# Kernel optimization log

Hardware: AMD Instinct MI355X
Metric: run time of the kernel (lower is better)

Reference implementation:

```python
import jax, jax.numpy as jnp
import numpy as np

B, C, H, W = 4, 64, 128, 128
HEADS, DIM_HEAD = 8, 64
INNER = HEADS * DIM_HEAD
EPS = 1e-12  # torch F.normalize default eps


def setup_inputs() -> dict:
    key = jax.random.key(0)
    ks = jax.random.split(key, 6)
    s_in = 1.0 / np.sqrt(C)
    s_pr = 1.0 / np.sqrt(INNER)
    return {
        "x_in": jax.random.normal(ks[0], (B, C, H, W), dtype=jnp.float32),
        "Wq": jax.random.uniform(ks[1], (C, INNER), jnp.float32, -s_in, s_in),
        "Wk": jax.random.uniform(ks[2], (C, INNER), jnp.float32, -s_in, s_in),
        "Wv": jax.random.uniform(ks[3], (C, INNER), jnp.float32, -s_in, s_in),
        "Wp": jax.random.uniform(ks[4], (INNER, C), jnp.float32, -s_pr, s_pr),
        "bp": jax.random.uniform(ks[5], (C,), jnp.float32, -s_pr, s_pr),
        "rescale": jnp.ones((HEADS, 1, 1), dtype=jnp.float32),
    }


def _l2norm(t):
    # normalize along last axis (the token axis n), matching F.normalize(p=2)
    n = jnp.sqrt(jnp.sum(t * t, axis=-1, keepdims=True))
    return t / jnp.maximum(n, EPS)


def reference(x_in, Wq, Wk, Wv, Wp, bp, rescale):
    b, c, h, w = x_in.shape
    n = h * w
    x = x_in.transpose(0, 2, 3, 1).reshape(b, n, c)  # [b, n, c]

    def heads_first(t):  # [b, n, inner] -> [b, heads, d, n]
        return t.reshape(b, n, HEADS, DIM_HEAD).transpose(0, 2, 3, 1)

    q = _l2norm(heads_first(x @ Wq))  # [b, H, d, n]
    k = _l2norm(heads_first(x @ Wk))
    v = heads_first(x @ Wv)

    # channel-channel attention: attn[d, e] = sum_n k[d, n] * q[e, n]
    attn = jnp.einsum('bhdn,bhen->bhde', k, q) * rescale  # [b, H, d, d]
    attn = jax.nn.softmax(attn, axis=-1)

    o = jnp.einsum('bhde,bhen->bhdn', attn, v)            # [b, H, d, n]
    o = o.transpose(0, 3, 1, 2).reshape(b, n, INNER)      # [b, n, inner]
    out = (o @ Wp + bp).reshape(b, h, w, c).transpose(0, 3, 1, 2)  # [b, c, h, w]
    return out, attn
```

## Files before the change

kernel.cpp:

```cpp
#include <hip/hip_runtime.h>
#include <math.h>

#define BB 4
#define CC 64
#define NN 16384
#define HEADS 8
#define INNER 512

__global__ __launch_bounds__(256) void k_gram(const float* __restrict__ x,
                                              float* __restrict__ part,
                                              int nslice) {
    const int s = blockIdx.x, b = blockIdx.y;
    const int t = threadIdx.x;
    const int g = t >> 6, lane = t & 63;
    const int rg = lane >> 4;
    const int r0 = g * 16 + rg * 4;
    const int c0 = (lane & 15) * 4;
    __shared__ float xs[64][68];
    float acc[4][4];
#pragma unroll
    for (int i = 0; i < 4; i++)
#pragma unroll
        for (int j = 0; j < 4; j++) acc[i][j] = 0.f;

    const float* xb = x + (size_t)b * CC * NN;
    const int cols = NN / nslice;
    const int ntiles = cols >> 6;
    const int nbase = s * cols;
    for (int tile = 0; tile < ntiles; ++tile) {
        const int n0 = nbase + tile * 64;
#pragma unroll
        for (int k = 0; k < 4; k++) {
            int f = k * 256 + t;
            int c = f >> 4, j4 = f & 15;
            const float4 v = *reinterpret_cast<const float4*>(xb + (size_t)c * NN + n0 + j4 * 4);
            xs[j4 * 4 + 0][c] = v.x; xs[j4 * 4 + 1][c] = v.y;
            xs[j4 * 4 + 2][c] = v.z; xs[j4 * 4 + 3][c] = v.w;
        }
        __syncthreads();
#pragma unroll 8
        for (int n = 0; n < 64; ++n) {
            const float4 a4 = *reinterpret_cast<const float4*>(&xs[n][r0]);
            const float4 b4 = *reinterpret_cast<const float4*>(&xs[n][c0]);
            acc[0][0] = fmaf(a4.x, b4.x, acc[0][0]); acc[0][1] = fmaf(a4.x, b4.y, acc[0][1]);
            acc[0][2] = fmaf(a4.x, b4.z, acc[0][2]); acc[0][3] = fmaf(a4.x, b4.w, acc[0][3]);
            acc[1][0] = fmaf(a4.y, b4.x, acc[1][0]); acc[1][1] = fmaf(a4.y, b4.y, acc[1][1]);
            acc[1][2] = fmaf(a4.y, b4.z, acc[1][2]); acc[1][3] = fmaf(a4.y, b4.w, acc[1][3]);
            acc[2][0] = fmaf(a4.z, b4.x, acc[2][0]); acc[2][1] = fmaf(a4.z, b4.y, acc[2][1]);
            acc[2][2] = fmaf(a4.z, b4.z, acc[2][2]); acc[2][3] = fmaf(a4.z, b4.w, acc[2][3]);
            acc[3][0] = fmaf(a4.w, b4.x, acc[3][0]); acc[3][1] = fmaf(a4.w, b4.y, acc[3][1]);
            acc[3][2] = fmaf(a4.w, b4.z, acc[3][2]); acc[3][3] = fmaf(a4.w, b4.w, acc[3][3]);
        }
        __syncthreads();
    }
    float* p = part + (size_t)(b * nslice + s) * 4096;
#pragma unroll
    for (int i = 0; i < 4; i++) {
        float4 v; v.x = acc[i][0]; v.y = acc[i][1]; v.z = acc[i][2]; v.w = acc[i][3];
        *reinterpret_cast<float4*>(p + (r0 + i) * 64 + c0) = v;
    }
}

__global__ __launch_bounds__(256) void k_redG(const float* __restrict__ part,
                                              float* __restrict__ G,
                                              int nslice) {
    const int b = blockIdx.y;
    const int idx = blockIdx.x * 256 + threadIdx.x;
    const float* p = part + (size_t)b * nslice * 4096 + idx;
    float s0 = 0.f, s1 = 0.f, s2 = 0.f, s3 = 0.f;
    for (int s = 0; s < nslice; s += 4) {
        s0 += p[(size_t)s * 4096];
        s1 += p[(size_t)(s + 1) * 4096];
        s2 += p[(size_t)(s + 2) * 4096];
        s3 += p[(size_t)(s + 3) * 4096];
    }
    G[(size_t)b * 4096 + idx] = (s0 + s1) + (s2 + s3);
}

__global__ __launch_bounds__(256) void k_attn(const float* __restrict__ G,
                                              const float* __restrict__ Wq,
                                              const float* __restrict__ Wk,
                                              const float* __restrict__ Wv,
                                              const float* __restrict__ Wp,
                                              const float* __restrict__ rescale,
                                              float* __restrict__ attn_out,
                                              float* __restrict__ Mg) {
    const int bh = blockIdx.x;
    const int b = bh >> 3, h = bh & 7;
    const int t = threadIdx.x;
    const int ti = t >> 4, tj = t & 15;
    __shared__ float Gs[64][68], Ws[64][68], Ts[64][68];
    __shared__ float qn[64], kn[64];

    for (int k = 0; k < 16; k++) { int f = k * 256 + t; Gs[f >> 6][f & 63] = G[(size_t)b * 4096 + f]; }
    for (int k = 0; k < 16; k++) { int f = k * 256 + t; int c = f >> 6, e = f & 63;
        Ws[c][e] = Wq[(size_t)c * INNER + h * 64 + e]; }
    __syncthreads();

    {
        float acc[4][4] = {};
        for (int k2 = 0; k2 < 64; k2++) {
            const float4 a4 = *reinterpret_cast<const float4*>(&Gs[k2][ti * 4]);
            const float4 b4 = *reinterpret_cast<const float4*>(&Ws[k2][tj * 4]);
            float a[4] = {a4.x, a4.y, a4.z, a4.w}, bv[4] = {b4.x, b4.y, b4.z, b4.w};
#pragma unroll
            for (int i = 0; i < 4; i++)
#pragma unroll
                for (int j = 0; j < 4; j++) acc[i][j] = fmaf(a[i], bv[j], acc[i][j]);
        }
#pragma unroll
        for (int i = 0; i < 4; i++)
#pragma unroll
            for (int j = 0; j < 4; j++) Ts[ti * 4 + i][tj * 4 + j] = acc[i][j];
    }
    __syncthreads();
    if (t < 64) {
        float s = 0.f;
        for (int c = 0; c < 64; c++) s += Ws[c][t] * Ts[c][t];
        qn[t] = fmaxf(sqrtf(s), 1e-12f);
    }
    __syncthreads();
    for (int k = 0; k < 16; k++) { int f = k * 256 + t; int c = f >> 6, e = f & 63;
        Ws[c][e] = Wk[(size_t)c * INNER + h * 64 + e]; }
    __syncthreads();

    float S[4][4] = {};
    for (int k2 = 0; k2 < 64; k2++) {
        const float4 a4 = *reinterpret_cast<const float4*>(&Ws[k2][ti * 4]);
        const float4 b4 = *reinterpret_cast<const float4*>(&Ts[k2][tj * 4]);
        float a[4] = {a4.x, a4.y, a4.z, a4.w}, bv[4] = {b4.x, b4.y, b4.z, b4.w};
#pragma unroll
        for (int i = 0; i < 4; i++)
#pragma unroll
            for (int j = 0; j < 4; j++) S[i][j] = fmaf(a[i], bv[j], S[i][j]);
    }

    {
        float acc[4][4] = {};
        for (int k2 = 0; k2 < 64; k2++) {
            const float4 a4 = *reinterpret_cast<const float4*>(&Gs[k2][ti * 4]);
            const float4 b4 = *reinterpret_cast<const float4*>(&Ws[k2][tj * 4]);
            float a[4] = {a4.x, a4.y, a4.z, a4.w}, bv[4] = {b4.x, b4.y, b4.z, b4.w};
#pragma unroll
            for (int i = 0; i < 4; i++)
#pragma unroll
                for (int j = 0; j < 4; j++) acc[i][j] = fmaf(a[i], bv[j], acc[i][j]);
        }
        __syncthreads();
#pragma unroll
        for (int i = 0; i < 4; i++)
#pragma unroll
            for (int j = 0; j < 4; j++) Ts[ti * 4 + i][tj * 4 + j] = acc[i][j];
    }
    __syncthreads();
    if (t < 64) {
        float s = 0.f;
        for (int c = 0; c < 64; c++) s += Ws[c][t] * Ts[c][t];
        kn[t] = fmaxf(sqrtf(s), 1e-12f);
    }
    __syncthreads();

    const float resc = rescale[h];
    float qinv[4];
#pragma unroll
    for (int j = 0; j < 4; j++) qinv[j] = 1.f / qn[tj * 4 + j];
    float p[4][4];
#pragma unroll
    for (int i = 0; i < 4; i++) {
        const float ki = resc / kn[ti * 4 + i];
        float m = -3.402823466e+38f;
#pragma unroll
        for (int j = 0; j < 4; j++) {
            float L = S[i][j] * ki * qinv[j];
            p[i][j] = L;
            m = fmaxf(m, L);
        }
        for (int o = 1; o < 16; o <<= 1) m = fmaxf(m, __shfl_xor(m, o, 64));
        float ssum = 0.f;
#pragma unroll
        for (int j = 0; j < 4; j++) { p[i][j] = expf(p[i][j] - m); ssum += p[i][j]; }
        for (int o = 1; o < 16; o <<= 1) ssum += __shfl_xor(ssum, o, 64);
        const float inv = 1.f / ssum;
#pragma unroll
        for (int j = 0; j < 4; j++) p[i][j] *= inv;
    }

    float* ao = attn_out + (size_t)bh * 64 * 64;
#pragma unroll
    for (int i = 0; i < 4; i++) {
        float4 v; v.x = p[i][0]; v.y = p[i][1]; v.z = p[i][2]; v.w = p[i][3];
        *reinterpret_cast<float4*>(ao + (size_t)(ti * 4 + i) * 64 + tj * 4) = v;
#pragma unroll
        for (int j = 0; j < 4; j++) Ts[tj * 4 + j][ti * 4 + i] = p[i][j];
    }
    for (int k = 0; k < 16; k++) { int f = k * 256 + t; int c = f >> 6, e = f & 63;
        Ws[e][c] = Wv[(size_t)c * INNER + h * 64 + e]; }
    __syncthreads();

    float accv[4][4] = {};
    for (int e = 0; e < 64; e++) {
        const float4 a4 = *reinterpret_cast<const float4*>(&Ws[e][ti * 4]);
        const float4 b4 = *reinterpret_cast<const float4*>(&Ts[e][tj * 4]);
        float a[4] = {a4.x, a4.y, a4.z, a4.w}, bv[4] = {b4.x, b4.y, b4.z, b4.w};
#pragma unroll
        for (int i = 0; i < 4; i++)
#pragma unroll
            for (int j = 0; j < 4; j++) accv[i][j] = fmaf(a[i], bv[j], accv[i][j]);
    }
    __syncthreads();
#pragma unroll
    for (int i = 0; i < 4; i++)
#pragma unroll
        for (int j = 0; j < 4; j++) Ts[tj * 4 + j][ti * 4 + i] = accv[i][j];
    for (int k = 0; k < 16; k++) { int f = k * 256 + t;
        Ws[f >> 6][f & 63] = Wp[(size_t)h * 4096 + f]; }
    __syncthreads();

    float accm[4][4] = {};
    for (int d = 0; d < 64; d++) {
        const float4 a4 = *reinterpret_cast<const float4*>(&Ts[d][ti * 4]);
        const float4 b4 = *reinterpret_cast<const float4*>(&Ws[d][tj * 4]);
        float a[4] = {a4.x, a4.y, a4.z, a4.w}, bv[4] = {b4.x, b4.y, b4.z, b4.w};
#pragma unroll
        for (int i = 0; i < 4; i++)
#pragma unroll
            for (int j = 0; j < 4; j++) accm[i][j] = fmaf(a[i], bv[j], accm[i][j]);
    }
    float* Mb = Mg + (size_t)b * 4096;
#pragma unroll
    for (int i = 0; i < 4; i++)
#pragma unroll
        for (int j = 0; j < 4; j++)
            atomicAdd(&Mb[(ti * 4 + i) * 64 + tj * 4 + j], accm[i][j]);
}

__global__ __launch_bounds__(256) void k_out(const float* __restrict__ x,
                                             const float* __restrict__ Mg,
                                             const float* __restrict__ bp,
                                             float* __restrict__ out) {
    const int sn = blockIdx.x, b = blockIdx.y;
    const int t = threadIdx.x, ti = t >> 4, tj = t & 15;
    __shared__ float Ms[64][68], xs[64][68];
    for (int k = 0; k < 16; k++) { int f = k * 256 + t; Ms[f >> 6][f & 63] = Mg[(size_t)b * 4096 + f]; }
    const int n0 = sn * 64;
    const float* xb = x + (size_t)b * CC * NN;
#pragma unroll
    for (int k = 0; k < 4; k++) {
        int f = k * 256 + t; int c = f >> 4, j4 = f & 15;
        float4 v = *reinterpret_cast<const float4*>(xb + (size_t)c * NN + n0 + j4 * 4);
        xs[c][j4 * 4 + 0] = v.x; xs[c][j4 * 4 + 1] = v.y;
        xs[c][j4 * 4 + 2] = v.z; xs[c][j4 * 4 + 3] = v.w;
    }
    __syncthreads();
    float acc[4][4];
#pragma unroll
    for (int i = 0; i < 4; i++) {
        const float bv = bp[ti * 4 + i];
#pragma unroll
        for (int j = 0; j < 4; j++) acc[i][j] = bv;
    }
    for (int c = 0; c < 64; c++) {
        const float4 m4 = *reinterpret_cast<const float4*>(&Ms[c][ti * 4]);
        const float4 x4 = *reinterpret_cast<const float4*>(&xs[c][tj * 4]);
        float m[4] = {m4.x, m4.y, m4.z, m4.w}, xv[4] = {x4.x, x4.y, x4.z, x4.w};
#pragma unroll
        for (int i = 0; i < 4; i++)
#pragma unroll
            for (int j = 0; j < 4; j++) acc[i][j] = fmaf(m[i], xv[j], acc[i][j]);
    }
    float* ob = out + (size_t)b * CC * NN;
#pragma unroll
    for (int i = 0; i < 4; i++) {
        float4 v; v.x = acc[i][0]; v.y = acc[i][1]; v.z = acc[i][2]; v.w = acc[i][3];
        *reinterpret_cast<float4*>(ob + (size_t)(ti * 4 + i) * NN + n0 + tj * 4) = v;
    }
}

extern "C" void kernel_launch(void* const* d_in, const int* in_sizes, int n_in,
                              void* d_out, int out_size, void* d_ws, size_t ws_size,
                              hipStream_t stream) {
    const float* x  = (const float*)d_in[0];
    const float* Wq = (const float*)d_in[1];
    const float* Wk = (const float*)d_in[2];
    const float* Wv = (const float*)d_in[3];
    const float* Wp = (const float*)d_in[4];
    const float* bp = (const float*)d_in[5];
    const float* rescale = (const float*)d_in[6];
    float* out = (float*)d_out;
    float* attn_out = out + (size_t)BB * CC * NN;
    float* ws = (float*)d_ws;

    const size_t fixed_floats = (size_t)BB * 4096
                              + (size_t)BB * 4096;
    int nslice = 256;
    while (nslice > 4 &&
           ((size_t)BB * nslice * 4096 + fixed_floats) * sizeof(float) > ws_size)
        nslice >>= 1;

    float* part = ws;
    float* G    = part + (size_t)BB * nslice * 4096;
    float* Mg   = G + (size_t)BB * 4096;

    hipMemsetAsync(Mg, 0, (size_t)BB * 4096 * sizeof(float), stream);
    hipLaunchKernelGGL(k_gram,  dim3(nslice, BB),  dim3(256), 0, stream, x, part, nslice);
    hipLaunchKernelGGL(k_redG,  dim3(16, BB),      dim3(256), 0, stream, part, G, nslice);
    hipLaunchKernelGGL(k_attn,  dim3(BB * HEADS),  dim3(256), 0, stream, G, Wq, Wk, Wv, Wp, rescale, attn_out, Mg);
    hipLaunchKernelGGL(k_out,   dim3(NN / 64, BB), dim3(256), 0, stream, x, Mg, bp, out);
}
```

Measured before the change: 137.6 us.

## Fold Gram reduction into atomics and split attention blocks by row quarter

The Gram kernel now uses a fixed 64 slices per batch and accumulates its partial results straight into G with atomicAdd, which removes the partial buffer and the separate reduction kernel. The attention kernel is split four ways per (batch, head): each block computes 16 rows of the attention matrix and their share of the fused Wv·attn·Wp product, then adds that share into M atomically. Weights are loaded up front with vectorized loads. This cuts a launch and the workspace traffic and gives 128 attention blocks instead of 32, in exchange for redundant Tq/Gs work per quarter, more atomic contention, and a Gram sum order that is no longer deterministic.

New measurement: 143.2 us. +4.1%, slower.

```diff
diff --git a/kernel.cpp b/kernel.cpp
--- a/kernel.cpp
+++ b/kernel.cpp
@@ -6,10 +6,10 @@
 #define NN 16384
 #define HEADS 8
 #define INNER 512
+#define NSLICE 64
 
 __global__ __launch_bounds__(256) void k_gram(const float* __restrict__ x,
-                                              float* __restrict__ part,
-                                              int nslice) {
+                                              float* __restrict__ G) {
     const int s = blockIdx.x, b = blockIdx.y;
     const int t = threadIdx.x;
     const int g = t >> 6, lane = t & 63;
@@ -24,10 +24,8 @@
         for (int j = 0; j < 4; j++) acc[i][j] = 0.f;
 
     const float* xb = x + (size_t)b * CC * NN;
-    const int cols = NN / nslice;
-    const int ntiles = cols >> 6;
-    const int nbase = s * cols;
-    for (int tile = 0; tile < ntiles; ++tile) {
+    const int nbase = s * (NN / NSLICE);
+    for (int tile = 0; tile < (NN / NSLICE) / 64; ++tile) {
         const int n0 = nbase + tile * 64;
 #pragma unroll
         for (int k = 0; k < 4; k++) {
@@ -53,28 +51,12 @@
         }
         __syncthreads();
     }
-    float* p = part + (size_t)(b * nslice + s) * 4096;
-#pragma unroll
-    for (int i = 0; i < 4; i++) {
-        float4 v; v.x = acc[i][0]; v.y = acc[i][1]; v.z = acc[i][2]; v.w = acc[i][3];
-        *reinterpret_cast<float4*>(p + (r0 + i) * 64 + c0) = v;
-    }
-}
-
-__global__ __launch_bounds__(256) void k_redG(const float* __restrict__ part,
-                                              float* __restrict__ G,
-                                              int nslice) {
-    const int b = blockIdx.y;
-    const int idx = blockIdx.x * 256 + threadIdx.x;
-    const float* p = part + (size_t)b * nslice * 4096 + idx;
-    float s0 = 0.f, s1 = 0.f, s2 = 0.f, s3 = 0.f;
-    for (int s = 0; s < nslice; s += 4) {
-        s0 += p[(size_t)s * 4096];
-        s1 += p[(size_t)(s + 1) * 4096];
-        s2 += p[(size_t)(s + 2) * 4096];
-        s3 += p[(size_t)(s + 3) * 4096];
-    }
-    G[(size_t)b * 4096 + idx] = (s0 + s1) + (s2 + s3);
+    float* Gb = G + (size_t)b * 4096;
+#pragma unroll
+    for (int i = 0; i < 4; i++)
+#pragma unroll
+        for (int j = 0; j < 4; j++)
+            atomicAdd(&Gb[(r0 + i) * 64 + c0 + j], acc[i][j]);
 }
 
 __global__ __launch_bounds__(256) void k_attn(const float* __restrict__ G,
@@ -85,18 +67,48 @@
                                               const float* __restrict__ rescale,
                                               float* __restrict__ attn_out,
                                               float* __restrict__ Mg) {
-    const int bh = blockIdx.x;
+    const int quad = blockIdx.x & 3;
+    const int bh = blockIdx.x >> 2;
     const int b = bh >> 3, h = bh & 7;
+    const int d0g = quad * 16;
     const int t = threadIdx.x;
+
+    __shared__ float Gs[64][68];
+    __shared__ float Tq[64][68];
+    __shared__ float Ws[64][68];
+    __shared__ float WkQ[64][20];
+    __shared__ float Atn[64][20];
+    __shared__ float qn[64], kn[16];
+
+#pragma unroll
+    for (int k = 0; k < 4; k++) {
+        int idx = k * 1024 + t * 4;
+        int r = idx >> 6, c = idx & 63;
+        float4 v = *reinterpret_cast<const float4*>(G + (size_t)b * 4096 + idx);
+        *reinterpret_cast<float4*>(&Gs[r][c]) = v;
+        float4 w = *reinterpret_cast<const float4*>(Wq + (size_t)r * INNER + h * 64 + c);
+        *reinterpret_cast<float4*>(&Ws[r][c]) = w;
+    }
+    {
+        int c = t >> 2, dl = (t & 3) * 4;
+        float4 v = *reinterpret_cast<const float4*>(Wk + (size_t)c * INNER + h * 64 + d0g + dl);
+        *reinterpret_cast<float4*>(&WkQ[c][dl]) = v;
+    }
+    float4 wvr[4];
+#pragma unroll
+    for (int k = 0; k < 4; k++) {
+        int idx = k * 1024 + t * 4;
+        int r = idx >> 6, c = idx & 63;
+        wvr[k] = *reinterpret_cast<const float4*>(Wv + (size_t)r * INNER + h * 64 + c);
+    }
+    float4 wpr;
+    {
+        int dl = t >> 4, c2 = (t & 15) * 4;
+        wpr = *reinterpret_cast<const float4*>(Wp + (size_t)(h * 64 + d0g + dl) * 64 + c2);
+    }
+    __syncthreads();
+
     const int ti = t >> 4, tj = t & 15;
-    __shared__ float Gs[64][68], Ws[64][68], Ts[64][68];
-    __shared__ float qn[64], kn[64];
-
-    for (int k = 0; k < 16; k++) { int f = k * 256 + t; Gs[f >> 6][f & 63] = G[(size_t)b * 4096 + f]; }
-    for (int k = 0; k < 16; k++) { int f = k * 256 + t; int c = f >> 6, e = f & 63;
-        Ws[c][e] = Wq[(size_t)c * INNER + h * 64 + e]; }
-    __syncthreads();
-
     {
         float acc[4][4] = {};
         for (int k2 = 0; k2 < 64; k2++) {
@@ -109,129 +121,121 @@
                 for (int j = 0; j < 4; j++) acc[i][j] = fmaf(a[i], bv[j], acc[i][j]);
         }
 #pragma unroll
-        for (int i = 0; i < 4; i++)
-#pragma unroll
-            for (int j = 0; j < 4; j++) Ts[ti * 4 + i][tj * 4 + j] = acc[i][j];
-    }
-    __syncthreads();
+        for (int i = 0; i < 4; i++) {
+            float4 v; v.x = acc[i][0]; v.y = acc[i][1]; v.z = acc[i][2]; v.w = acc[i][3];
+            *reinterpret_cast<float4*>(&Tq[ti * 4 + i][tj * 4]) = v;
+        }
+    }
+    {
+        const int c = t >> 2, dl0 = (t & 3) * 4;
+        float tk[4] = {};
+        for (int k = 0; k < 64; k++) {
+            const float a = Gs[k][c];
+            const float4 b4 = *reinterpret_cast<const float4*>(&WkQ[k][dl0]);
+            tk[0] = fmaf(a, b4.x, tk[0]); tk[1] = fmaf(a, b4.y, tk[1]);
+            tk[2] = fmaf(a, b4.z, tk[2]); tk[3] = fmaf(a, b4.w, tk[3]);
+        }
+        float4 v; v.x = tk[0]; v.y = tk[1]; v.z = tk[2]; v.w = tk[3];
+        *reinterpret_cast<float4*>(&Atn[c][dl0]) = v;
+    }
+    __syncthreads();
+
+    {
+        const int e = t >> 2, sub = t & 3;
+        float s = 0.f;
+        for (int c = sub * 16; c < sub * 16 + 16; c++) s += Ws[c][e] * Tq[c][e];
+        s += __shfl_xor(s, 1, 64);
+        s += __shfl_xor(s, 2, 64);
+        if (sub == 0) qn[e] = fmaxf(sqrtf(s), 1e-12f);
+    }
     if (t < 64) {
+        const int dl = t >> 2, sub = t & 3;
         float s = 0.f;
-        for (int c = 0; c < 64; c++) s += Ws[c][t] * Ts[c][t];
-        qn[t] = fmaxf(sqrtf(s), 1e-12f);
-    }
-    __syncthreads();
-    for (int k = 0; k < 16; k++) { int f = k * 256 + t; int c = f >> 6, e = f & 63;
-        Ws[c][e] = Wk[(size_t)c * INNER + h * 64 + e]; }
-    __syncthreads();
-
-    float S[4][4] = {};
-    for (int k2 = 0; k2 < 64; k2++) {
-        const float4 a4 = *reinterpret_cast<const float4*>(&Ws[k2][ti * 4]);
-        const float4 b4 = *reinterpret_cast<const float4*>(&Ts[k2][tj * 4]);
-        float a[4] = {a4.x, a4.y, a4.z, a4.w}, bv[4] = {b4.x, b4.y, b4.z, b4.w};
-#pragma unroll
-        for (int i = 0; i < 4; i++)
-#pragma unroll
-            for (int j = 0; j < 4; j++) S[i][j] = fmaf(a[i], bv[j], S[i][j]);
-    }
-
-    {
-        float acc[4][4] = {};
-        for (int k2 = 0; k2 < 64; k2++) {
-            const float4 a4 = *reinterpret_cast<const float4*>(&Gs[k2][ti * 4]);
-            const float4 b4 = *reinterpret_cast<const float4*>(&Ws[k2][tj * 4]);
-            float a[4] = {a4.x, a4.y, a4.z, a4.w}, bv[4] = {b4.x, b4.y, b4.z, b4.w};
-#pragma unroll
-            for (int i = 0; i < 4; i++)
-#pragma unroll
-                for (int j = 0; j < 4; j++) acc[i][j] = fmaf(a[i], bv[j], acc[i][j]);
-        }
-        __syncthreads();
-#pragma unroll
-        for (int i = 0; i < 4; i++)
-#pragma unroll
-            for (int j = 0; j < 4; j++) Ts[ti * 4 + i][tj * 4 + j] = acc[i][j];
-    }
-    __syncthreads();
-    if (t < 64) {
-        float s = 0.f;
-        for (int c = 0; c < 64; c++) s += Ws[c][t] * Ts[c][t];
-        kn[t] = fmaxf(sqrtf(s), 1e-12f);
+        for (int c = sub * 16; c < sub * 16 + 16; c++) s += WkQ[c][dl] * Atn[c][dl];
+        s += __shfl_xor(s, 1, 64);
+        s += __shfl_xor(s, 2, 64);
+        if (sub == 0) kn[dl] = fmaxf(sqrtf(s), 1e-12f);
+    }
+    const int d = t >> 4, e0 = (t & 15) * 4;
+    float s4[4] = {};
+    for (int c = 0; c < 64; c++) {
+        const float a = WkQ[c][d];
+        const float4 b4 = *reinterpret_cast<const float4*>(&Tq[c][e0]);
+        s4[0] = fmaf(a, b4.x, s4[0]); s4[1] = fmaf(a, b4.y, s4[1]);
+        s4[2] = fmaf(a, b4.z, s4[2]); s4[3] = fmaf(a, b4.w, s4[3]);
     }
     __syncthreads();
 
     const float resc = rescale[h];
-    float qinv[4];
-#pragma unroll
-    for (int j = 0; j < 4; j++) qinv[j] = 1.f / qn[tj * 4 + j];
-    float p[4][4];
-#pragma unroll
-    for (int i = 0; i < 4; i++) {
-        const float ki = resc / kn[ti * 4 + i];
+    float p[4];
+    {
+        const float ki = resc / kn[d];
         float m = -3.402823466e+38f;
 #pragma unroll
         for (int j = 0; j < 4; j++) {
-            float L = S[i][j] * ki * qinv[j];
-            p[i][j] = L;
-            m = fmaxf(m, L);
+            p[j] = s4[j] * ki / qn[e0 + j];
+            m = fmaxf(m, p[j]);
         }
         for (int o = 1; o < 16; o <<= 1) m = fmaxf(m, __shfl_xor(m, o, 64));
         float ssum = 0.f;
 #pragma unroll
-        for (int j = 0; j < 4; j++) { p[i][j] = expf(p[i][j] - m); ssum += p[i][j]; }
+        for (int j = 0; j < 4; j++) { p[j] = expf(p[j] - m); ssum += p[j]; }
         for (int o = 1; o < 16; o <<= 1) ssum += __shfl_xor(ssum, o, 64);
         const float inv = 1.f / ssum;
 #pragma unroll
-        for (int j = 0; j < 4; j++) p[i][j] *= inv;
-    }
-
-    float* ao = attn_out + (size_t)bh * 64 * 64;
-#pragma unroll
-    for (int i = 0; i < 4; i++) {
-        float4 v; v.x = p[i][0]; v.y = p[i][1]; v.z = p[i][2]; v.w = p[i][3];
-        *reinterpret_cast<float4*>(ao + (size_t)(ti * 4 + i) * 64 + tj * 4) = v;
-#pragma unroll
-        for (int j = 0; j < 4; j++) Ts[tj * 4 + j][ti * 4 + i] = p[i][j];
-    }
-    for (int k = 0; k < 16; k++) { int f = k * 256 + t; int c = f >> 6, e = f & 63;
-        Ws[e][c] = Wv[(size_t)c * INNER + h * 64 + e]; }
-    __syncthreads();
-
-    float accv[4][4] = {};
-    for (int e = 0; e < 64; e++) {
-        const float4 a4 = *reinterpret_cast<const float4*>(&Ws[e][ti * 4]);
-        const float4 b4 = *reinterpret_cast<const float4*>(&Ts[e][tj * 4]);
-        float a[4] = {a4.x, a4.y, a4.z, a4.w}, bv[4] = {b4.x, b4.y, b4.z, b4.w};
+        for (int j = 0; j < 4; j++) p[j] *= inv;
+    }
+    {
+        float4 v; v.x = p[0]; v.y = p[1]; v.z = p[2]; v.w = p[3];
+        *reinterpret_cast<float4*>(attn_out + (size_t)bh * 4096 + (size_t)(d0g + d) * 64 + e0) = v;
+#pragma unroll
+        for (int j = 0; j < 4; j++) Atn[e0 + j][d] = p[j];
+    }
+#pragma unroll
+    for (int k = 0; k < 4; k++) {
+        int idx = k * 1024 + t * 4;
+        int r = idx >> 6, c = idx & 63;
+        *reinterpret_cast<float4*>(&Ws[r][c]) = wvr[k];
+    }
+    {
+        int dl = t >> 4, c2 = (t & 15) * 4;
+        *reinterpret_cast<float4*>(&Tq[16 + dl][c2]) = wpr;
+    }
+    __syncthreads();
+
+    {
+        const int c = t >> 2, dl0 = (t & 3) * 4;
+        float wv4[4] = {};
+        for (int e = 0; e < 64; e++) {
+            const float a = Ws[c][e];
+            const float4 b4 = *reinterpret_cast<const float4*>(&Atn[e][dl0]);
+            wv4[0] = fmaf(a, b4.x, wv4[0]); wv4[1] = fmaf(a, b4.y, wv4[1]);
+            wv4[2] = fmaf(a, b4.z, wv4[2]); wv4[3] = fmaf(a, b4.w, wv4[3]);
+        }
+#pragma unroll
+        for (int j = 0; j < 4; j++) Tq[dl0 + j][c] = wv4[j];
+    }
+    __syncthreads();
+
+    {
+        float acc[4][4] = {};
+#pragma unroll
+        for (int dl = 0; dl < 16; dl++) {
+            const float4 a4 = *reinterpret_cast<const float4*>(&Tq[dl][ti * 4]);
+            const float4 b4 = *reinterpret_cast<const float4*>(&Tq[16 + dl][tj * 4]);
+            float a[4] = {a4.x, a4.y, a4.z, a4.w}, bv[4] = {b4.x, b4.y, b4.z, b4.w};
+#pragma unroll
+            for (int i = 0; i < 4; i++)
+#pragma unroll
+                for (int j = 0; j < 4; j++) acc[i][j] = fmaf(a[i], bv[j], acc[i][j]);
+        }
+        float* Mb = Mg + (size_t)b * 4096;
 #pragma unroll
         for (int i = 0; i < 4; i++)
 #pragma unroll
-            for (int j = 0; j < 4; j++) accv[i][j] = fmaf(a[i], bv[j], accv[i][j]);
-    }
-    __syncthreads();
-#pragma unroll
-    for (int i = 0; i < 4; i++)
-#pragma unroll
-        for (int j = 0; j < 4; j++) Ts[tj * 4 + j][ti * 4 + i] = accv[i][j];
-    for (int k = 0; k < 16; k++) { int f = k * 256 + t;
-        Ws[f >> 6][f & 63] = Wp[(size_t)h * 4096 + f]; }
-    __syncthreads();
-
-    float accm[4][4] = {};
-    for (int d = 0; d < 64; d++) {
-        const float4 a4 = *reinterpret_cast<const float4*>(&Ts[d][ti * 4]);
-        const float4 b4 = *reinterpret_cast<const float4*>(&Ws[d][tj * 4]);
-        float a[4] = {a4.x, a4.y, a4.z, a4.w}, bv[4] = {b4.x, b4.y, b4.z, b4.w};
-#pragma unroll
-        for (int i = 0; i < 4; i++)
-#pragma unroll
-            for (int j = 0; j < 4; j++) accm[i][j] = fmaf(a[i], bv[j], accm[i][j]);
-    }
-    float* Mb = Mg + (size_t)b * 4096;
-#pragma unroll
-    for (int i = 0; i < 4; i++)
-#pragma unroll
-        for (int j = 0; j < 4; j++)
-            atomicAdd(&Mb[(ti * 4 + i) * 64 + tj * 4 + j], accm[i][j]);
+            for (int j = 0; j < 4; j++)
+                atomicAdd(&Mb[(ti * 4 + i) * 64 + tj * 4 + j], acc[i][j]);
+    }
 }
 
 __global__ __launch_bounds__(256) void k_out(const float* __restrict__ x,
@@ -290,20 +294,11 @@
     float* attn_out = out + (size_t)BB * CC * NN;
     float* ws = (float*)d_ws;
 
-    const size_t fixed_floats = (size_t)BB * 4096
-                              + (size_t)BB * 4096;
-    int nslice = 256;
-    while (nslice > 4 &&
-           ((size_t)BB * nslice * 4096 + fixed_floats) * sizeof(float) > ws_size)
-        nslice >>= 1;
-
-    float* part = ws;
-    float* G    = part + (size_t)BB * nslice * 4096;
-    float* Mg   = G + (size_t)BB * 4096;
-
-    hipMemsetAsync(Mg, 0, (size_t)BB * 4096 * sizeof(float), stream);
-    hipLaunchKernelGGL(k_gram,  dim3(nslice, BB),  dim3(256), 0, stream, x, part, nslice);
-    hipLaunchKernelGGL(k_redG,  dim3(16, BB),      dim3(256), 0, stream, part, G, nslice);
-    hipLaunchKernelGGL(k_attn,  dim3(BB * HEADS),  dim3(256), 0, stream, G, Wq, Wk, Wv, Wp, rescale, attn_out, Mg);
-    hipLaunchKernelGGL(k_out,   dim3(NN / 64, BB), dim3(256), 0, stream, x, Mg, bp, out);
+    float* G  = ws;
+    float* Mg = G + (size_t)BB * 4096;
+
+    hipMemsetAsync(G, 0, (size_t)BB * 4096 * 2 * sizeof(float), stream);
+    hipLaunchKernelGGL(k_gram, dim3(NSLICE, BB),      dim3(256), 0, stream, x, G);
+    hipLaunchKernelGGL(k_attn, dim3(BB * HEADS * 4),  dim3(256), 0, stream, G, Wq, Wk, Wv, Wp, rescale, attn_out, Mg);
+    hipLaunchKernelGGL(k_out,  dim3(NN / 64, BB),     dim3(256), 0, stream, x, Mg, bp, out);
 }
```
